# Optimization experiments

Measured on AMD Instinct MI355X. Metric: run time of the kernel, lower is better.

The kernel has to match this reference:

```python
import jax, jax.numpy as jnp
import numpy as np

# ultralytics ops.non_max_suppression defaults
CONF_THRES = 0.25
IOU_THRES = 0.45
MAX_DET = 300          # max detections returned per image
MAX_WH = 7680.0        # class-offset constant for class-aware NMS
MAX_NMS = 1024         # fixed candidate cap (ultralytics uses 30000; fixed-size for jit)


def _xywh2xyxy(x):
    # x: [..., 4] (cx, cy, w, h) -> (x1, y1, x2, y2)
    xy, half_wh = x[..., :2], x[..., 2:] * 0.5
    return jnp.concatenate([xy - half_wh, xy + half_wh], axis=-1)


def _pairwise_iou(b):
    # b: [K, 4] xyxy -> [K, K] IoU
    area = (b[:, 2] - b[:, 0]) * (b[:, 3] - b[:, 1])
    lt = jnp.maximum(b[:, None, :2], b[None, :, :2])
    rb = jnp.minimum(b[:, None, 2:], b[None, :, 2:])
    wh = jnp.clip(rb - lt, 0.0)
    inter = wh[..., 0] * wh[..., 1]
    return inter / (area[:, None] + area[None, :] - inter + 1e-7)


def _nms_single(pred):
    # pred: [4+nc, N] raw detector output for one image
    boxes = _xywh2xyxy(pred[:4].T)          # [N, 4]
    scores = pred[4:].T                     # [N, nc]
    conf = scores.max(axis=-1)              # [N]
    cls = scores.argmax(axis=-1).astype(pred.dtype)  # [N]

    valid = conf > CONF_THRES
    masked_conf = jnp.where(valid, conf, -1.0)
    top_conf, idx = jax.lax.top_k(masked_conf, MAX_NMS)   # sorted desc
    b = boxes[idx]                          # [K, 4]
    c = cls[idx]                            # [K]

    # class-aware NMS via coordinate offset per class
    iou = _pairwise_iou(b + c[:, None] * MAX_WH)          # [K, K]

    keep0 = top_conf > CONF_THRES
    ar = jnp.arange(MAX_NMS)

    def body(i, keep):
        # greedy: if box i is kept, suppress all lower-scored boxes with high IoU
        sup = keep[i] & (iou[i] > IOU_THRES) & (ar > i)
        return keep & ~sup

    keep = jax.lax.fori_loop(0, MAX_NMS, body, keep0)

    kept_conf = jnp.where(keep, top_conf, -1.0)
    det_conf, di = jax.lax.top_k(kept_conf, MAX_DET)
    det = jnp.concatenate(
        [b[di], det_conf[:, None], c[di][:, None]], axis=-1)  # [MAX_DET, 6]
    ok = (det_conf > CONF_THRES)[:, None]
    return jnp.where(ok, det, 0.0)


def setup_inputs() -> dict:
    key = jax.random.key(0)
    # [batch, 4+nc, num_anchors]: xywh in [0,1), class scores in [0,1)
    preds = jax.random.uniform(key, (32, 84, 8400), dtype=jnp.float32)
    return {"preds": preds}


def reference(preds):
    dets = jax.vmap(_nms_single)(preds)  # [B, MAX_DET, 6] (xyxy, conf, cls)
    return dets[0]                       # module returns preds[0]
```

## Files before the change

### kernel.cpp

```cpp
#include <hip/hip_runtime.h>
#include <cstdint>
#include <cstddef>


#define NA    8400
#define NCLS  80
#define NTOP  1024
#define NDET  300
#define CONF_T 0.25f
#define IOU_T  0.45f
#define MAXWH  7680.0f

#define NSLICE 25
#define SLICEW 336

#define OFF_KEY   0
#define OFF_CLS   33600
#define OFF_CONF  67200
#define OFF_SCONF 100800
#define OFF_SX1   104896
#define OFF_SY1   108992
#define OFF_SX2   113088
#define OFF_SY2   117184
#define OFF_SCLS  121280
#define OFF_SUP   125376
#define OFF_RANK  256448

typedef unsigned long long u64;
typedef unsigned int u32;

__device__ __forceinline__ int sw(int j) { return j + (j >> 6); }

__device__ __forceinline__ u32 f2mono(float f) {
    u32 u = __float_as_uint(f);
    return u ^ ((u & 0x80000000u) ? 0xFFFFFFFFu : 0x80000000u);
}
__device__ __forceinline__ float mono2f(u32 m) {
    u32 u = (m & 0x80000000u) ? (m ^ 0x80000000u) : ~m;
    return __uint_as_float(u);
}
__device__ __forceinline__ u64 rl64(u64 v, int g) {
    u32 lo = (u32)__builtin_amdgcn_readlane((int)(u32)v, g);
    u32 hi = (u32)__builtin_amdgcn_readlane((int)(u32)(v >> 32), g);
    return ((u64)hi << 32) | lo;
}

__global__ __launch_bounds__(1024) void k_confcls(const float* __restrict__ pred,
                                                  u32* __restrict__ key,
                                                  float* __restrict__ clsf,
                                                  float* __restrict__ conf,
                                                  u32* __restrict__ rank)
{
    __shared__ u64 pk[4][256];
    int tid = threadIdx.x;
    int q = tid >> 8, t = tid & 255;
    int a = blockIdx.x * 256 + t;
    u64 pv = 0ULL;
    if (a < NA) {
        const float* s = pred + 4 * NA + (size_t)(q * 20) * NA;
        float best = s[a];
        int bc = q * 20;
#pragma unroll
        for (int c = 1; c < 20; ++c) {
            float v = s[(size_t)c * NA + a];
            if (v > best) { best = v; bc = q * 20 + c; }
        }
        pv = ((u64)f2mono(best) << 32) | (u32)(255 - bc);
    }
    pk[q][t] = pv;
    __syncthreads();
    if (q == 0 && a < NA) {
        u64 m0 = pk[0][t], m1 = pk[1][t], m2 = pk[2][t], m3 = pk[3][t];
        u64 mm = m0 > m1 ? m0 : m1;
        u64 nn = m2 > m3 ? m2 : m3;
        if (nn > mm) mm = nn;
        float best = mono2f((u32)(mm >> 32));
        int bc = 255 - (int)(mm & 0xFFu);
        float m = (best > CONF_T) ? best : -1.0f;
        key[a]  = ~f2mono(m);
        clsf[a] = (float)bc;
        conf[a] = m;
        rank[a] = 0u;
    }
}

__global__ __launch_bounds__(256) void k_rank_partial(const u32* __restrict__ key,
                                                      u32* __restrict__ rank)
{
    __shared__ __align__(16) u32 kh[SLICEW];
    int tid = threadIdx.x;
    int s   = blockIdx.y;
    int jb  = s * SLICEW;
    for (int k = tid; k < SLICEW; k += 256) kh[k] = key[jb + k];
    __syncthreads();

    int a = blockIdx.x * 256 + tid;
    if (a >= NA) return;

    u64 myk = (((u64)key[a]) << 32) | (u32)a;
    u32 r = 0;
    const uint4* kv4 = (const uint4*)kh;
#pragma unroll 4
    for (int j4 = 0; j4 < SLICEW / 4; ++j4) {
        uint4 kk = kv4[j4];
        u32 j = (u32)jb + (u32)j4 * 4u;
        r += ((((u64)kk.x) << 32) | (j + 0u)) < myk;
        r += ((((u64)kk.y) << 32) | (j + 1u)) < myk;
        r += ((((u64)kk.z) << 32) | (j + 2u)) < myk;
        r += ((((u64)kk.w) << 32) | (j + 3u)) < myk;
    }
    atomicAdd(&rank[a], r);
}

__global__ __launch_bounds__(256) void k_scatter(const float* __restrict__ pred,
                                                 const u32* __restrict__ rank,
                                                 const float* __restrict__ clsf,
                                                 const float* __restrict__ conf,
                                                 float* __restrict__ wsf)
{
    int a = blockIdx.x * 256 + threadIdx.x;
    if (a >= NA) return;
    u32 r = rank[a];
    if (r < NTOP) {
#pragma clang fp contract(off)
        float x = pred[0 * NA + a], y = pred[1 * NA + a];
        float w = pred[2 * NA + a], h = pred[3 * NA + a];
        float hw = w * 0.5f, hh = h * 0.5f;
        wsf[OFF_SCONF / 4 + r] = conf[a];
        wsf[OFF_SX1  / 4 + r] = x - hw;
        wsf[OFF_SY1  / 4 + r] = y - hh;
        wsf[OFF_SX2  / 4 + r] = x + hw;
        wsf[OFF_SY2  / 4 + r] = y + hh;
        wsf[OFF_SCLS / 4 + r] = clsf[a];
    }
}

__global__ __launch_bounds__(256) void k_supmat(const float* __restrict__ wsf,
                                                u64* __restrict__ sup)
{
#pragma clang fp contract(off)
    __shared__ float ox1[NTOP + 16], oy1[NTOP + 16];
    __shared__ float ox2[NTOP + 16], oy2[NTOP + 16];
    __shared__ float oar[NTOP + 16];
    int tid = threadIdx.x;
    for (int k = tid; k < NTOP; k += 256) {
        float cls = wsf[OFF_SCLS / 4 + k];
        float off = cls * MAXWH;
        float x1 = wsf[OFF_SX1 / 4 + k] + off;
        float y1 = wsf[OFF_SY1 / 4 + k] + off;
        float x2 = wsf[OFF_SX2 / 4 + k] + off;
        float y2 = wsf[OFF_SY2 / 4 + k] + off;
        int si = sw(k);
        ox1[si] = x1; oy1[si] = y1; ox2[si] = x2; oy2[si] = y2;
        oar[si] = (x2 - x1) * (y2 - y1);
    }
    __syncthreads();

    int gid = blockIdx.x * 256 + tid;
    int i = gid >> 4;
    int l = gid & 15;
    int si = sw(i);
    float bx1 = ox1[si], by1 = oy1[si], bx2 = ox2[si], by2 = oy2[si], ba = oar[si];
    u64 bits = 0ULL;
    int j0 = l << 6;
#pragma unroll 4
    for (int jj = 0; jj < 64; ++jj) {
        int j = j0 + jj;
        int sj = sw(j);
        float xx1 = fmaxf(bx1, ox1[sj]);
        float yy1 = fmaxf(by1, oy1[sj]);
        float xx2 = fminf(bx2, ox2[sj]);
        float yy2 = fminf(by2, oy2[sj]);
        float w  = fmaxf(xx2 - xx1, 0.0f);
        float hh = fmaxf(yy2 - yy1, 0.0f);
        float inter = w * hh;
        float denom = ba + oar[sj] - inter + 1e-7f;
        bool s = (j > i) && ((inter / denom) > IOU_T);
        bits |= ((u64)s) << jj;
    }
    sup[(size_t)i * 16 + l] = bits;
}

__global__ __launch_bounds__(512) void k_nms_out(const float* __restrict__ wsf,
                                                 const u64* __restrict__ sup,
                                                 float* __restrict__ out)
{
    __shared__ u64 kc[16];
    __shared__ u32 pcs[16];
    int tid  = threadIdx.x;
    int lane = tid & 63;
    int wv   = tid >> 6;

    const float* sconf = wsf + OFF_SCONF / 4;
    u64 b1 = __ballot(sconf[tid] > CONF_T);
    u64 b2 = __ballot(sconf[512 + tid] > CONF_T);
    if (lane == 0) { kc[wv] = b1; kc[8 + wv] = b2; }
    __syncthreads();

    if (wv == 0 && lane < 16) {
        int l = lane;
        u64 keep = kc[l];
        u64 cur = 0ULL;
        u64 A[16], B[16];
#pragma unroll
        for (int k = 0; k < 16; ++k) A[k] = sup[(size_t)k * 16 + l];

        for (int m2 = 0; m2 < 32; ++m2) {
            int m = m2 * 2;
#pragma unroll
            for (int k = 0; k < 16; ++k) B[k] = sup[(size_t)((m + 1) * 16 + k) * 16 + l];
            {
                int g = m >> 2;
                if ((m & 3) == 0) cur = rl64(keep, g);
                u64 rg[16];
#pragma unroll
                for (int k = 0; k < 16; ++k) rg[k] = rl64(A[k], g);
#pragma unroll
                for (int k = 0; k < 16; ++k) {
                    int ii = ((m & 3) << 4) + k;
                    u64 sel = 0ULL - ((cur >> ii) & 1ULL);
                    keep &= ~(A[k] & sel);
                    cur  &= ~(rg[k] & sel);
                }
            }
            if (m2 < 31) {
#pragma unroll
                for (int k = 0; k < 16; ++k) A[k] = sup[(size_t)((m + 2) * 16 + k) * 16 + l];
            }
            {
                int mb = m + 1;
                int g = mb >> 2;
                u64 rg[16];
#pragma unroll
                for (int k = 0; k < 16; ++k) rg[k] = rl64(B[k], g);
#pragma unroll
                for (int k = 0; k < 16; ++k) {
                    int ii = ((mb & 3) << 4) + k;
                    u64 sel = 0ULL - ((cur >> ii) & 1ULL);
                    keep &= ~(B[k] & sel);
                    cur  &= ~(rg[k] & sel);
                }
            }
        }
        kc[l] = keep;
    }
    __syncthreads();

    if (tid < 16) pcs[tid] = (u32)__popcll(kc[tid]);
    __syncthreads();

    if (tid < NDET) {
        int acc = 0, chunk = -1, off = 0;
#pragma unroll
        for (int c = 0; c < 16; ++c) {
            int p = (int)pcs[c];
            if (chunk < 0 && tid < acc + p) { chunk = c; off = tid - acc; }
            acc += p;
        }
        float o0 = 0.f, o1 = 0.f, o2 = 0.f, o3 = 0.f, o4 = 0.f, o5 = 0.f;
        if (chunk >= 0) {
            u64 mk = kc[chunk];
            for (int q = 0; q < off; ++q) mk &= mk - 1ULL;
            int p = chunk * 64 + __builtin_ctzll(mk);
            o0 = wsf[OFF_SX1  / 4 + p];
            o1 = wsf[OFF_SY1  / 4 + p];
            o2 = wsf[OFF_SX2  / 4 + p];
            o3 = wsf[OFF_SY2  / 4 + p];
            o4 = wsf[OFF_SCONF / 4 + p];
            o5 = wsf[OFF_SCLS / 4 + p];
        }
        out[tid * 6 + 0] = o0; out[tid * 6 + 1] = o1; out[tid * 6 + 2] = o2;
        out[tid * 6 + 3] = o3; out[tid * 6 + 4] = o4; out[tid * 6 + 5] = o5;
    }
}

extern "C" void kernel_launch(void* const* d_in, const int* in_sizes, int n_in,
                              void* d_out, int out_size, void* d_ws, size_t ws_size,
                              hipStream_t stream)
{
    const float* preds = (const float*)d_in[0];
    char* ws = (char*)d_ws;
    u32* key    = (u32*)(ws + OFF_KEY);
    float* clsf = (float*)(ws + OFF_CLS);
    float* conf = (float*)(ws + OFF_CONF);
    float* wsf  = (float*)ws;
    u64* sup    = (u64*)(ws + OFF_SUP);
    u32* rank   = (u32*)(ws + OFF_RANK);
    float* out  = (float*)d_out;

    hipLaunchKernelGGL(k_confcls,      dim3(33),         dim3(1024), 0, stream, preds, key, clsf, conf, rank);
    hipLaunchKernelGGL(k_rank_partial, dim3(33, NSLICE), dim3(256),  0, stream, key, rank);
    hipLaunchKernelGGL(k_scatter,      dim3(33),         dim3(256),  0, stream, preds, rank, clsf, conf, wsf);
    hipLaunchKernelGGL(k_supmat,       dim3(64),         dim3(256),  0, stream, wsf, sup);
    hipLaunchKernelGGL(k_nms_out,      dim3(1),          dim3(512),  0, stream, wsf, sup, out);
}
```

Measured before the change: 173.3 us.

## Fuse rank and scatter via last-block ticket, stage sup in LDS, skip empty NMS groups

Merges the rank and scatter kernels using an atomic ticket, so the last finishing block does the scatter and one launch is removed. Also splits the class argmax across 8 row groups over more blocks, packs box coordinates into float4 in LDS for supmat with smaller blocks, and copies the suppression matrix into LDS before the serial NMS loop. The NMS loop now skips 16-row groups whose keep bits are all zero. The cost is that the scatter runs serially in a single block, and the 128 KB LDS buffer may limit occupancy, though only one block runs there anyway.

```diff
diff --git a/kernel.cpp b/kernel.cpp
--- a/kernel.cpp
+++ b/kernel.cpp
@@ -25,6 +25,7 @@
 #define OFF_SCLS  121280
 #define OFF_SUP   125376
 #define OFF_RANK  256448
+#define OFF_DONE  290048
 
 typedef unsigned long long u64;
 typedef unsigned int u32;
@@ -49,31 +50,31 @@
                                                   u32* __restrict__ key,
                                                   float* __restrict__ clsf,
                                                   float* __restrict__ conf,
-                                                  u32* __restrict__ rank)
-{
-    __shared__ u64 pk[4][256];
+                                                  u32* __restrict__ rank,
+                                                  u32* __restrict__ done)
+{
+    __shared__ u64 pk[8][128];
     int tid = threadIdx.x;
-    int q = tid >> 8, t = tid & 255;
-    int a = blockIdx.x * 256 + t;
+    int q = tid >> 7, t = tid & 127;
+    int a = blockIdx.x * 128 + t;
     u64 pv = 0ULL;
     if (a < NA) {
-        const float* s = pred + 4 * NA + (size_t)(q * 20) * NA;
+        const float* s = pred + (size_t)(4 + q * 10) * NA;
         float best = s[a];
-        int bc = q * 20;
-#pragma unroll
-        for (int c = 1; c < 20; ++c) {
+        int bc = q * 10;
+#pragma unroll
+        for (int c = 1; c < 10; ++c) {
             float v = s[(size_t)c * NA + a];
-            if (v > best) { best = v; bc = q * 20 + c; }
+            if (v > best) { best = v; bc = q * 10 + c; }
         }
         pv = ((u64)f2mono(best) << 32) | (u32)(255 - bc);
     }
     pk[q][t] = pv;
     __syncthreads();
     if (q == 0 && a < NA) {
-        u64 m0 = pk[0][t], m1 = pk[1][t], m2 = pk[2][t], m3 = pk[3][t];
-        u64 mm = m0 > m1 ? m0 : m1;
-        u64 nn = m2 > m3 ? m2 : m3;
-        if (nn > mm) mm = nn;
+        u64 mm = pk[0][t];
+#pragma unroll
+        for (int r = 1; r < 8; ++r) { u64 v = pk[r][t]; if (v > mm) mm = v; }
         float best = mono2f((u32)(mm >> 32));
         int bc = 255 - (int)(mm & 0xFFu);
         float m = (best > CONF_T) ? best : -1.0f;
@@ -82,12 +83,19 @@
         conf[a] = m;
         rank[a] = 0u;
     }
-}
-
-__global__ __launch_bounds__(256) void k_rank_partial(const u32* __restrict__ key,
-                                                      u32* __restrict__ rank)
+    if (blockIdx.x == 0 && tid == 0) *done = 0u;
+}
+
+__global__ __launch_bounds__(256) void k_rank_scatter(const u32* __restrict__ key,
+                                                      u32* __restrict__ rank,
+                                                      const float* __restrict__ pred,
+                                                      const float* __restrict__ clsf,
+                                                      const float* __restrict__ conf,
+                                                      float* __restrict__ wsf,
+                                                      u32* __restrict__ done)
 {
     __shared__ __align__(16) u32 kh[SLICEW];
+    __shared__ int tick;
     int tid = threadIdx.x;
     int s   = blockIdx.y;
     int jb  = s * SLICEW;
@@ -95,55 +103,55 @@
     __syncthreads();
 
     int a = blockIdx.x * 256 + tid;
-    if (a >= NA) return;
-
-    u64 myk = (((u64)key[a]) << 32) | (u32)a;
-    u32 r = 0;
-    const uint4* kv4 = (const uint4*)kh;
+    if (a < NA) {
+        u64 myk = (((u64)key[a]) << 32) | (u32)a;
+        u32 r = 0;
+        const uint4* kv4 = (const uint4*)kh;
 #pragma unroll 4
-    for (int j4 = 0; j4 < SLICEW / 4; ++j4) {
-        uint4 kk = kv4[j4];
-        u32 j = (u32)jb + (u32)j4 * 4u;
-        r += ((((u64)kk.x) << 32) | (j + 0u)) < myk;
-        r += ((((u64)kk.y) << 32) | (j + 1u)) < myk;
-        r += ((((u64)kk.z) << 32) | (j + 2u)) < myk;
-        r += ((((u64)kk.w) << 32) | (j + 3u)) < myk;
-    }
-    atomicAdd(&rank[a], r);
-}
-
-__global__ __launch_bounds__(256) void k_scatter(const float* __restrict__ pred,
-                                                 const u32* __restrict__ rank,
-                                                 const float* __restrict__ clsf,
-                                                 const float* __restrict__ conf,
-                                                 float* __restrict__ wsf)
-{
-    int a = blockIdx.x * 256 + threadIdx.x;
-    if (a >= NA) return;
-    u32 r = rank[a];
-    if (r < NTOP) {
+        for (int j4 = 0; j4 < SLICEW / 4; ++j4) {
+            uint4 kk = kv4[j4];
+            u32 j = (u32)jb + (u32)j4 * 4u;
+            r += ((((u64)kk.x) << 32) | (j + 0u)) < myk;
+            r += ((((u64)kk.y) << 32) | (j + 1u)) < myk;
+            r += ((((u64)kk.z) << 32) | (j + 2u)) < myk;
+            r += ((((u64)kk.w) << 32) | (j + 3u)) < myk;
+        }
+        atomicAdd(&rank[a], r);
+    }
+    __syncthreads();
+    if (tid == 0) {
+        __threadfence();
+        tick = (int)atomicAdd(done, 1u);
+    }
+    __syncthreads();
+    if (tick == 33 * NSLICE - 1) {
+        __threadfence();
+        for (int a2 = tid; a2 < NA; a2 += 256) {
+            u32 r = atomicAdd(&rank[a2], 0u);
+            if (r < NTOP) {
 #pragma clang fp contract(off)
-        float x = pred[0 * NA + a], y = pred[1 * NA + a];
-        float w = pred[2 * NA + a], h = pred[3 * NA + a];
-        float hw = w * 0.5f, hh = h * 0.5f;
-        wsf[OFF_SCONF / 4 + r] = conf[a];
-        wsf[OFF_SX1  / 4 + r] = x - hw;
-        wsf[OFF_SY1  / 4 + r] = y - hh;
-        wsf[OFF_SX2  / 4 + r] = x + hw;
-        wsf[OFF_SY2  / 4 + r] = y + hh;
-        wsf[OFF_SCLS / 4 + r] = clsf[a];
-    }
-}
-
-__global__ __launch_bounds__(256) void k_supmat(const float* __restrict__ wsf,
+                float x = pred[0 * NA + a2], y = pred[1 * NA + a2];
+                float w = pred[2 * NA + a2], h = pred[3 * NA + a2];
+                float hw = w * 0.5f, hh = h * 0.5f;
+                wsf[OFF_SCONF / 4 + r] = conf[a2];
+                wsf[OFF_SX1  / 4 + r] = x - hw;
+                wsf[OFF_SY1  / 4 + r] = y - hh;
+                wsf[OFF_SX2  / 4 + r] = x + hw;
+                wsf[OFF_SY2  / 4 + r] = y + hh;
+                wsf[OFF_SCLS / 4 + r] = clsf[a2];
+            }
+        }
+    }
+}
+
+__global__ __launch_bounds__(128) void k_supmat(const float* __restrict__ wsf,
                                                 u64* __restrict__ sup)
 {
 #pragma clang fp contract(off)
-    __shared__ float ox1[NTOP + 16], oy1[NTOP + 16];
-    __shared__ float ox2[NTOP + 16], oy2[NTOP + 16];
-    __shared__ float oar[NTOP + 16];
+    __shared__ float4 obox[NTOP + 16];
+    __shared__ float  oar[NTOP + 16];
     int tid = threadIdx.x;
-    for (int k = tid; k < NTOP; k += 256) {
+    for (int k = tid; k < NTOP; k += 128) {
         float cls = wsf[OFF_SCLS / 4 + k];
         float off = cls * MAXWH;
         float x1 = wsf[OFF_SX1 / 4 + k] + off;
@@ -151,26 +159,28 @@
         float x2 = wsf[OFF_SX2 / 4 + k] + off;
         float y2 = wsf[OFF_SY2 / 4 + k] + off;
         int si = sw(k);
-        ox1[si] = x1; oy1[si] = y1; ox2[si] = x2; oy2[si] = y2;
-        oar[si] = (x2 - x1) * (y2 - y1);
-    }
-    __syncthreads();
-
-    int gid = blockIdx.x * 256 + tid;
+        obox[si] = make_float4(x1, y1, x2, y2);
+        oar[si]  = (x2 - x1) * (y2 - y1);
+    }
+    __syncthreads();
+
+    int gid = blockIdx.x * 128 + tid;
     int i = gid >> 4;
     int l = gid & 15;
     int si = sw(i);
-    float bx1 = ox1[si], by1 = oy1[si], bx2 = ox2[si], by2 = oy2[si], ba = oar[si];
+    float4 bb = obox[si];
+    float  ba = oar[si];
     u64 bits = 0ULL;
     int j0 = l << 6;
 #pragma unroll 4
     for (int jj = 0; jj < 64; ++jj) {
         int j = j0 + jj;
         int sj = sw(j);
-        float xx1 = fmaxf(bx1, ox1[sj]);
-        float yy1 = fmaxf(by1, oy1[sj]);
-        float xx2 = fminf(bx2, ox2[sj]);
-        float yy2 = fminf(by2, oy2[sj]);
+        float4 ob = obox[sj];
+        float xx1 = fmaxf(bb.x, ob.x);
+        float yy1 = fmaxf(bb.y, ob.y);
+        float xx2 = fminf(bb.z, ob.z);
+        float yy2 = fminf(bb.w, ob.w);
         float w  = fmaxf(xx2 - xx1, 0.0f);
         float hh = fmaxf(yy2 - yy1, 0.0f);
         float inter = w * hh;
@@ -185,12 +195,19 @@
                                                  const u64* __restrict__ sup,
                                                  float* __restrict__ out)
 {
+    __shared__ u64 lsup[NTOP * 16];
     __shared__ u64 kc[16];
     __shared__ u32 pcs[16];
     int tid  = threadIdx.x;
     int lane = tid & 63;
     int wv   = tid >> 6;
 
+    {
+        const uint4* gs = (const uint4*)sup;
+        uint4* lv = (uint4*)lsup;
+        for (int idx = tid; idx < NTOP * 8; idx += 512) lv[idx] = gs[idx];
+    }
+
     const float* sconf = wsf + OFF_SCONF / 4;
     u64 b1 = __ballot(sconf[tid] > CONF_T);
     u64 b2 = __ballot(sconf[512 + tid] > CONF_T);
@@ -203,42 +220,42 @@
         u64 cur = 0ULL;
         u64 A[16], B[16];
 #pragma unroll
-        for (int k = 0; k < 16; ++k) A[k] = sup[(size_t)k * 16 + l];
-
-        for (int m2 = 0; m2 < 32; ++m2) {
-            int m = m2 * 2;
-#pragma unroll
-            for (int k = 0; k < 16; ++k) B[k] = sup[(size_t)((m + 1) * 16 + k) * 16 + l];
-            {
-                int g = m >> 2;
-                if ((m & 3) == 0) cur = rl64(keep, g);
-                u64 rg[16];
-#pragma unroll
-                for (int k = 0; k < 16; ++k) rg[k] = rl64(A[k], g);
-#pragma unroll
-                for (int k = 0; k < 16; ++k) {
-                    int ii = ((m & 3) << 4) + k;
-                    u64 sel = 0ULL - ((cur >> ii) & 1ULL);
-                    keep &= ~(A[k] & sel);
-                    cur  &= ~(rg[k] & sel);
+        for (int k = 0; k < 16; ++k) A[k] = lsup[k * 16 + l];
+
+        for (int m = 0; m < 64; ++m) {
+            if (m < 63) {
+                if (m & 1) {
+#pragma unroll
+                    for (int k = 0; k < 16; ++k) A[k] = lsup[((m + 1) * 16 + k) * 16 + l];
+                } else {
+#pragma unroll
+                    for (int k = 0; k < 16; ++k) B[k] = lsup[((m + 1) * 16 + k) * 16 + l];
                 }
             }
-            if (m2 < 31) {
-#pragma unroll
-                for (int k = 0; k < 16; ++k) A[k] = sup[(size_t)((m + 2) * 16 + k) * 16 + l];
-            }
-            {
-                int mb = m + 1;
-                int g = mb >> 2;
+            int g = m >> 2;
+            if ((m & 3) == 0) cur = rl64(keep, g);
+            int sh = (m & 3) << 4;
+            u32 f16 = (u32)((cur >> sh) & 0xFFFFu);
+            if (f16) {
                 u64 rg[16];
-#pragma unroll
-                for (int k = 0; k < 16; ++k) rg[k] = rl64(B[k], g);
-#pragma unroll
-                for (int k = 0; k < 16; ++k) {
-                    int ii = ((mb & 3) << 4) + k;
-                    u64 sel = 0ULL - ((cur >> ii) & 1ULL);
-                    keep &= ~(B[k] & sel);
-                    cur  &= ~(rg[k] & sel);
+                if (m & 1) {
+#pragma unroll
+                    for (int k = 0; k < 16; ++k) rg[k] = rl64(B[k], g);
+#pragma unroll
+                    for (int k = 0; k < 16; ++k) {
+                        u64 sel = 0ULL - ((cur >> (sh + k)) & 1ULL);
+                        keep &= ~(B[k] & sel);
+                        cur  &= ~(rg[k] & sel);
+                    }
+                } else {
+#pragma unroll
+                    for (int k = 0; k < 16; ++k) rg[k] = rl64(A[k], g);
+#pragma unroll
+                    for (int k = 0; k < 16; ++k) {
+                        u64 sel = 0ULL - ((cur >> (sh + k)) & 1ULL);
+                        keep &= ~(A[k] & sel);
+                        cur  &= ~(rg[k] & sel);
+                    }
                 }
             }
         }
@@ -286,11 +303,11 @@
     float* wsf  = (float*)ws;
     u64* sup    = (u64*)(ws + OFF_SUP);
     u32* rank   = (u32*)(ws + OFF_RANK);
+    u32* done   = (u32*)(ws + OFF_DONE);
     float* out  = (float*)d_out;
 
-    hipLaunchKernelGGL(k_confcls,      dim3(33),         dim3(1024), 0, stream, preds, key, clsf, conf, rank);
-    hipLaunchKernelGGL(k_rank_partial, dim3(33, NSLICE), dim3(256),  0, stream, key, rank);
-    hipLaunchKernelGGL(k_scatter,      dim3(33),         dim3(256),  0, stream, preds, rank, clsf, conf, wsf);
-    hipLaunchKernelGGL(k_supmat,       dim3(64),         dim3(256),  0, stream, wsf, sup);
+    hipLaunchKernelGGL(k_confcls,      dim3(66),         dim3(1024), 0, stream, preds, key, clsf, conf, rank, done);
+    hipLaunchKernelGGL(k_rank_scatter, dim3(33, NSLICE), dim3(256),  0, stream, key, rank, preds, clsf, conf, wsf, done);
+    hipLaunchKernelGGL(k_supmat,       dim3(128),        dim3(128),  0, stream, wsf, sup);
     hipLaunchKernelGGL(k_nms_out,      dim3(1),          dim3(512),  0, stream, wsf, sup, out);
 }
```

After: 232.8 us. 1.34x slower.
